# Optimization experiments

Hardware: AMD Instinct MI355X
Metric: run time of the kernel (lower is better)

## Reference

```python
import jax, jax.numpy as jnp
import numpy as np

N_EMBD = 1024
N_HEAD = 16
HEAD = N_EMBD // N_HEAD
B, T = 4, 2048


def setup_inputs() -> dict:
    key = jax.random.key(0)
    k1, k2, k3, k4, k5 = jax.random.split(key, 5)
    s = 1.0 / np.sqrt(N_EMBD)
    x = jax.random.normal(k1, (B, T, N_EMBD), dtype=jnp.float32)
    W_qkv = jax.random.uniform(k2, (N_EMBD, 3 * N_EMBD), jnp.float32, -s, s)
    b_qkv = jax.random.uniform(k3, (3 * N_EMBD,), jnp.float32, -s, s)
    W_out = jax.random.uniform(k4, (N_EMBD, N_EMBD), jnp.float32, -s, s)
    b_out = jax.random.uniform(k5, (N_EMBD,), jnp.float32, -s, s)
    return {"x": x, "W_qkv": W_qkv, "b_qkv": b_qkv, "W_out": W_out, "b_out": b_out}


def reference(x, W_qkv, b_qkv, W_out, b_out):
    Bx, Tx, C = x.shape
    qkv = x @ W_qkv + b_qkv                      # [B,T,3C]
    q, k, v = jnp.split(qkv, 3, axis=-1)
    def to_heads(t):
        return t.reshape(Bx, Tx, N_HEAD, HEAD).transpose(0, 2, 1, 3)  # [B,H,T,hd]
    q, k, v = to_heads(q), to_heads(k), to_heads(v)
    scores = jnp.einsum('bhqd,bhkd->bhqk', q, k) / np.sqrt(HEAD)
    causal = jnp.tril(jnp.ones((Tx, Tx), dtype=bool))
    scores = jnp.where(causal[None, None, :, :], scores, jnp.float32(-1e9))
    attn = jax.nn.softmax(scores, axis=-1)       # dropout p=0 (eval)
    out = jnp.einsum('bhqk,bhkd->bhqd', attn, v)
    out = out.transpose(0, 2, 1, 3).reshape(Bx, Tx, C)
    return out @ W_out + b_out
```

## Files before the change

### kernel.cpp

```cpp
#include <hip/hip_runtime.h>

typedef __attribute__((ext_vector_type(8))) short short8;
typedef __attribute__((ext_vector_type(8))) _Float16 half8;
typedef __attribute__((ext_vector_type(4))) float f32x4;
typedef __attribute__((ext_vector_type(16))) float f32x16;

#define MFMA_BF16(a, b, c) __builtin_amdgcn_mfma_f32_16x16x32_bf16(a, b, c, 0, 0, 0)
#define MFMA32_BF16(a, b, c) __builtin_amdgcn_mfma_f32_32x32x16_bf16(a, b, c, 0, 0, 0)
#define MFMA32_F16(a, b, c) __builtin_amdgcn_mfma_f32_32x32x16_f16(a, b, c, 0, 0, 0)

#define GLD16(g, l)                                                          \
  __builtin_amdgcn_global_load_lds(                                          \
      (const __attribute__((address_space(1))) unsigned int*)(g),            \
      (__attribute__((address_space(3))) unsigned int*)(l), 16, 0, 0)

__device__ __forceinline__ unsigned short f2bf(float f) {
  unsigned int u = __float_as_uint(f);
  u += 0x7fffu + ((u >> 16) & 1u);
  return (unsigned short)(u >> 16);
}

__global__ __launch_bounds__(256) void cvt_f32_bf16_k(const float* __restrict__ in,
                                                      unsigned short* __restrict__ out,
                                                      int n4) {
  int i = blockIdx.x * 256 + threadIdx.x;
  if (i < n4) {
    float4 v = reinterpret_cast<const float4*>(in)[i];
    ushort4 o;
    o.x = f2bf(v.x); o.y = f2bf(v.y); o.z = f2bf(v.z); o.w = f2bf(v.w);
    reinterpret_cast<ushort4*>(out)[i] = o;
  }
}

__global__ __launch_bounds__(256) void transpose_cvt_k(const float* __restrict__ W,
                                                       unsigned short* __restrict__ Wt,
                                                       int N) {
  __shared__ float tile[64][65];
  const int tid = threadIdx.x;
  const int tk = blockIdx.x * 64;
  const int tn = blockIdx.y * 64;
#pragma unroll
  for (int c = 0; c < 4; ++c) {
    int k = c * 16 + (tid >> 4);
    int n = (tid & 15) * 4;
    float4 v = *reinterpret_cast<const float4*>(&W[(size_t)(tk + k) * N + tn + n]);
    tile[k][n] = v.x; tile[k][n + 1] = v.y; tile[k][n + 2] = v.z; tile[k][n + 3] = v.w;
  }
  __syncthreads();
#pragma unroll
  for (int p = 0; p < 2; ++p) {
    int n = p * 32 + (tid >> 3);
    int k = (tid & 7) * 8;
    ushort4 a, b;
    a.x = f2bf(tile[k + 0][n]); a.y = f2bf(tile[k + 1][n]);
    a.z = f2bf(tile[k + 2][n]); a.w = f2bf(tile[k + 3][n]);
    b.x = f2bf(tile[k + 4][n]); b.y = f2bf(tile[k + 5][n]);
    b.z = f2bf(tile[k + 6][n]); b.w = f2bf(tile[k + 7][n]);
    *reinterpret_cast<ushort4*>(&Wt[(size_t)(tn + n) * 1024 + tk + k]) = a;
    *reinterpret_cast<ushort4*>(&Wt[(size_t)(tn + n) * 1024 + tk + k + 4]) = b;
  }
}

template <int MODE, int BN>
__global__ __launch_bounds__(256) void gemm_bt(const unsigned short* __restrict__ A,
                                               const unsigned short* __restrict__ Bt,
                                               const float* __restrict__ bias,
                                               float* __restrict__ outF,
                                               unsigned short* __restrict__ q_ws,
                                               unsigned short* __restrict__ k_ws,
                                               unsigned short* __restrict__ vt_ws,
                                               int M, int N, int K) {
  constexpr int NJ = BN / 32;
  constexpr int NBC = BN * 64 / 2048;
  __shared__ unsigned short As[128 * 64];
  __shared__ unsigned short Bs[BN * 64];

  const int tid = threadIdx.x;
  const int wave = tid >> 6, lane = tid & 63;
  const int quad = lane >> 4, l15 = lane & 15;
  const int m0 = blockIdx.x * 128, n0 = blockIdx.y * BN;
  const int wm = (wave & 1) * 64, wn = (wave >> 1) * (BN / 2);

  const f32x4 zf = {0.f, 0.f, 0.f, 0.f};
  f32x4 acc[4][NJ];
#pragma unroll
  for (int i = 0; i < 4; ++i)
#pragma unroll
    for (int j = 0; j < NJ; ++j) acc[i][j] = zf;

  const int rr = tid >> 3;
  const int scol = ((tid & 7) ^ (rr & 7)) * 8;
  const int swz = l15 & 7;

  for (int kt = 0; kt < K; kt += 64) {
    __syncthreads();
#pragma unroll
    for (int c = 0; c < 4; ++c)
      GLD16(&A[(size_t)(m0 + c * 32 + rr) * K + kt + scol], &As[c * 2048 + tid * 8]);
#pragma unroll
    for (int c = 0; c < NBC; ++c)
      GLD16(&Bt[(size_t)(n0 + c * 32 + rr) * K + kt + scol], &Bs[c * 2048 + tid * 8]);
    __syncthreads();

#pragma unroll
    for (int kk = 0; kk < 2; ++kk) {
      const int ch = (kk * 4 + quad) ^ swz;
      short8 af[4], bg[NJ];
#pragma unroll
      for (int i = 0; i < 4; ++i)
        af[i] = *reinterpret_cast<const short8*>(&As[(wm + i * 16 + l15) * 64 + ch * 8]);
#pragma unroll
      for (int j = 0; j < NJ; ++j)
        bg[j] = *reinterpret_cast<const short8*>(&Bs[(wn + j * 16 + l15) * 64 + ch * 8]);
#pragma unroll
      for (int i = 0; i < 4; ++i)
#pragma unroll
        for (int j = 0; j < NJ; ++j) acc[i][j] = MFMA_BF16(af[i], bg[j], acc[i][j]);
    }
  }

  const float kScQ = 0.125f * 1.44269504088896f;
  const int cls = n0 >> 10;
#pragma unroll
  for (int i = 0; i < 4; ++i) {
#pragma unroll
    for (int j = 0; j < NJ; ++j) {
      const int n = n0 + wn + j * 16 + l15;
      const float bv = bias[n];
      const int mb = m0 + wm + i * 16 + quad * 4;
      if (MODE == 1) {
#pragma unroll
        for (int r = 0; r < 4; ++r) outF[(size_t)(mb + r) * N + n] = acc[i][j][r] + bv;
      } else if (cls == 0) {
        const int b = mb >> 11, t0 = mb & 2047;
        const int h = n >> 6, d = n & 63;
#pragma unroll
        for (int r = 0; r < 4; ++r)
          q_ws[(((size_t)(b * 16 + h)) * 2048 + t0 + r) * 64 + d] =
              f2bf((acc[i][j][r] + bv) * kScQ);
      } else if (cls == 1) {
        const int b = mb >> 11, t0 = mb & 2047;
        const int n2 = n - 1024, h = n2 >> 6, d = n2 & 63;
#pragma unroll
        for (int r = 0; r < 4; ++r)
          k_ws[(((size_t)(b * 16 + h)) * 2048 + t0 + r) * 64 + d] = f2bf(acc[i][j][r] + bv);
      } else {
        const int b = mb >> 11, t0 = mb & 2047;
        const int n2 = n - 2048, h = n2 >> 6, d = n2 & 63;
        uint2 pk;
        pk.x = __builtin_bit_cast(unsigned int,
                                  __builtin_amdgcn_cvt_pkrtz(acc[i][j][0] + bv, acc[i][j][1] + bv));
        pk.y = __builtin_bit_cast(unsigned int,
                                  __builtin_amdgcn_cvt_pkrtz(acc[i][j][2] + bv, acc[i][j][3] + bv));
        *reinterpret_cast<uint2*>(
            &vt_ws[(((size_t)(b * 16 + h)) * 64 + d) * 2048 + t0]) = pk;
      }
    }
  }
}

__global__ __launch_bounds__(256, 3) void attn_k(const unsigned short* __restrict__ q_ws,
                                                 const unsigned short* __restrict__ k_ws,
                                                 const unsigned short* __restrict__ vt_ws,
                                                 unsigned short* __restrict__ att_ws) {
  const int T = 2048;
  const int bid = blockIdx.x;
  const int bh = (bid & 7) * 8 + ((bid >> 3) & 7);
  const int s = 15 - (bid >> 6);
  const int tid = threadIdx.x;
  const int wv = tid >> 6, lane = tid & 63;
  const int L = lane & 31, hl = lane >> 5;

  const unsigned short* Qh = q_ws + (size_t)bh * T * 64;
  const unsigned short* Kh = k_ws + (size_t)bh * T * 64;
  const _Float16* Vh = (const _Float16*)vt_ws + (size_t)bh * 64 * T;
  const int b = bh >> 4, h = bh & 15;

  __shared__ unsigned short Ks[2][64 * 64];
  __shared__ _Float16 Vs[2][64 * 64];
  __shared__ _Float16 plds_all[4][32 * 72];
  _Float16* plds = plds_all[wv];

  const int qw = s * 4 + wv;
  const int q0 = qw * 32;
  const int diagTile = qw >> 1;
  const int nk = 2 * s + 2;
  const int myq = q0 + L;

  short8 qb[4];
#pragma unroll
  for (int kk = 0; kk < 4; ++kk)
    qb[kk] = *reinterpret_cast<const short8*>(&Qh[(size_t)(q0 + L) * 64 + kk * 16 + hl * 8]);

  f32x16 o0 = {}, o1 = {};
  float l_i = 0.f;

  const int srow8 = tid >> 3;
  const int schunk = (tid & 7) ^ (srow8 & 7);

  GLD16(&Kh[(size_t)srow8 * 64 + schunk * 8], &Ks[0][tid * 8]);
  GLD16(&Kh[(size_t)(32 + srow8) * 64 + schunk * 8], &Ks[0][2048 + tid * 8]);
  GLD16(&Vh[(size_t)srow8 * T + schunk * 8], &Vs[0][tid * 8]);
  GLD16(&Vh[(size_t)(32 + srow8) * T + schunk * 8], &Vs[0][2048 + tid * 8]);

  for (int kt = 0; kt < nk; ++kt) {
    const int cur = kt & 1, nxt = cur ^ 1;
    if (kt) asm volatile("s_barrier" ::: "memory");
    const int pf = (kt + 1 < nk) ? kt + 1 : nk - 1;
    GLD16(&Kh[(size_t)(pf * 64 + srow8) * 64 + schunk * 8], &Ks[nxt][tid * 8]);
    GLD16(&Kh[(size_t)(pf * 64 + 32 + srow8) * 64 + schunk * 8], &Ks[nxt][2048 + tid * 8]);
    GLD16(&Vh[(size_t)srow8 * T + pf * 64 + schunk * 8], &Vs[nxt][tid * 8]);
    GLD16(&Vh[(size_t)(32 + srow8) * T + pf * 64 + schunk * 8], &Vs[nxt][2048 + tid * 8]);
    asm volatile("s_waitcnt vmcnt(4)\n\ts_barrier" ::: "memory");

    if (kt <= diagTile) {
      const unsigned short* KsC = Ks[cur];
      const _Float16* VsC = Vs[cur];
      const int kb = kt * 64;

      f32x16 sc0 = {}, sc1 = {};
#pragma unroll
      for (int kk = 0; kk < 4; ++kk) {
        const int sl = ((kk * 2 + hl) ^ (L & 7)) * 8;
        short8 k0 = *reinterpret_cast<const short8*>(&KsC[L * 64 + sl]);
        short8 k1 = *reinterpret_cast<const short8*>(&KsC[(32 + L) * 64 + sl]);
        sc0 = MFMA32_BF16(k0, qb[kk], sc0);
        sc1 = MFMA32_BF16(k1, qb[kk], sc1);
      }
      if (kt == diagTile) {
#pragma unroll
        for (int reg = 0; reg < 16; ++reg) {
          const int row = (reg & 3) + 8 * (reg >> 2) + 4 * hl;
          sc0[reg] = (kb + row > myq) ? -1e30f : sc0[reg];
          sc1[reg] = (kb + 32 + row > myq) ? -1e30f : sc1[reg];
        }
      }
#pragma unroll
      for (int c = 0; c < 2; ++c) {
        const f32x16& scc = c ? sc1 : sc0;
#pragma unroll
        for (int g = 0; g < 4; ++g) {
          float a0 = exp2f(scc[4 * g + 0]);
          float a1 = exp2f(scc[4 * g + 1]);
          float a2 = exp2f(scc[4 * g + 2]);
          float a3 = exp2f(scc[4 * g + 3]);
          l_i += (a0 + a1) + (a2 + a3);
          uint2 pk;
          pk.x = __builtin_bit_cast(unsigned int, __builtin_amdgcn_cvt_pkrtz(a0, a1));
          pk.y = __builtin_bit_cast(unsigned int, __builtin_amdgcn_cvt_pkrtz(a2, a3));
          *reinterpret_cast<uint2*>(&plds[L * 72 + c * 32 + g * 8 + hl * 4]) = pk;
        }
      }
      asm volatile("" ::: "memory");

#pragma unroll
      for (int t = 0; t < 4; ++t) {
        half8 pb = *reinterpret_cast<const half8*>(&plds[L * 72 + t * 16 + hl * 8]);
        const int sl = ((t * 2 + hl) ^ (L & 7)) * 8;
        half8 v0 = *reinterpret_cast<const half8*>(&VsC[L * 64 + sl]);
        half8 v1 = *reinterpret_cast<const half8*>(&VsC[(32 + L) * 64 + sl]);
        o0 = MFMA32_F16(v0, pb, o0);
        o1 = MFMA32_F16(v1, pb, o1);
      }
      asm volatile("" ::: "memory");
    }
  }
  asm volatile("s_waitcnt vmcnt(0)" ::: "memory");

  l_i += __shfl_xor(l_i, 32);
  const float inv = 1.f / l_i;
#pragma unroll
  for (int sg = 0; sg < 2; ++sg) {
    const f32x16& oo = sg ? o1 : o0;
#pragma unroll
    for (int g = 0; g < 4; ++g) {
      const int d0 = sg * 32 + g * 8 + hl * 4;
      uint2 ov;
      ov.x = (unsigned)f2bf(oo[4 * g + 0] * inv) | ((unsigned)f2bf(oo[4 * g + 1] * inv) << 16);
      ov.y = (unsigned)f2bf(oo[4 * g + 2] * inv) | ((unsigned)f2bf(oo[4 * g + 3] * inv) << 16);
      *reinterpret_cast<uint2*>(
          &att_ws[(size_t)(b * 2048 + q0 + L) * 1024 + h * 64 + d0]) = ov;
    }
  }
}

extern "C" void kernel_launch(void* const* d_in, const int* in_sizes, int n_in,
                              void* d_out, int out_size, void* d_ws, size_t ws_size,
                              hipStream_t stream) {
  (void)in_sizes; (void)n_in; (void)out_size; (void)ws_size;
  const float* x     = (const float*)d_in[0];
  const float* W_qkv = (const float*)d_in[1];
  const float* b_qkv = (const float*)d_in[2];
  const float* W_out = (const float*)d_in[3];
  const float* b_out = (const float*)d_in[4];
  float* out = (float*)d_out;

  char* ws = (char*)d_ws;
  unsigned short* xb    = (unsigned short*)(ws);
  unsigned short* wqkvT = (unsigned short*)(ws + 16777216);
  unsigned short* woutT = (unsigned short*)(ws + 23068672);
  unsigned short* q_ws  = (unsigned short*)(ws + 25165824);
  unsigned short* k_ws  = (unsigned short*)(ws + 41943040);
  unsigned short* vt_ws = (unsigned short*)(ws + 58720256);
  unsigned short* attb  = (unsigned short*)(ws + 75497472);

  cvt_f32_bf16_k<<<8192, 256, 0, stream>>>(x, xb, 2097152);
  transpose_cvt_k<<<dim3(16, 48), 256, 0, stream>>>(W_qkv, wqkvT, 3072);
  transpose_cvt_k<<<dim3(16, 16), 256, 0, stream>>>(W_out, woutT, 1024);

  dim3 g1(64, 24);
  gemm_bt<0, 128><<<g1, 256, 0, stream>>>(xb, wqkvT, b_qkv, nullptr, q_ws, k_ws, vt_ws,
                                          8192, 3072, 1024);
  attn_k<<<1024, 256, 0, stream>>>(q_ws, k_ws, vt_ws, attb);

  dim3 g2(64, 16);
  gemm_bt<1, 64><<<g2, 256, 0, stream>>>(attb, woutT, b_out, out, nullptr, nullptr, nullptr,
                                         8192, 1024, 1024);
}
```

Measured before the change: 243.0 us.

## Double-buffer GEMM K-loop and replace attention P LDS roundtrip with permlane swaps

The GEMM now uses double-buffered LDS tiles with a K-step of 32. The next tile's global-to-LDS load is issued before computing on the current tile, synchronised with vmcnt waits and raw barriers, and launch bounds ask for 4 blocks per CU. In attention, the probability matrix no longer goes through a per-wave LDS scratch buffer. It is rearranged in registers with v_permlane32_swap to form the MFMA B operand, which frees LDS and allows 4 blocks per CU. The risks are tighter register budgets from the raised occupancy target and fragile hand-written vmcnt counts. The smaller K tile also drops the XOR swizzle, which may add LDS bank conflicts.

Result: slower. 255.2 us (+5.0%).

```diff
diff --git a/kernel.cpp b/kernel.cpp
--- a/kernel.cpp
+++ b/kernel.cpp
@@ -4,6 +4,7 @@
 typedef __attribute__((ext_vector_type(8))) _Float16 half8;
 typedef __attribute__((ext_vector_type(4))) float f32x4;
 typedef __attribute__((ext_vector_type(16))) float f32x16;
+typedef __attribute__((ext_vector_type(4))) unsigned int u32x4;
 
 #define MFMA_BF16(a, b, c) __builtin_amdgcn_mfma_f32_16x16x32_bf16(a, b, c, 0, 0, 0)
 #define MFMA32_BF16(a, b, c) __builtin_amdgcn_mfma_f32_32x32x16_bf16(a, b, c, 0, 0, 0)
@@ -62,18 +63,18 @@
 }
 
 template <int MODE, int BN>
-__global__ __launch_bounds__(256) void gemm_bt(const unsigned short* __restrict__ A,
-                                               const unsigned short* __restrict__ Bt,
-                                               const float* __restrict__ bias,
-                                               float* __restrict__ outF,
-                                               unsigned short* __restrict__ q_ws,
-                                               unsigned short* __restrict__ k_ws,
-                                               unsigned short* __restrict__ vt_ws,
-                                               int M, int N, int K) {
+__global__ __launch_bounds__(256, 4) void gemm_bt(const unsigned short* __restrict__ A,
+                                                  const unsigned short* __restrict__ Bt,
+                                                  const float* __restrict__ bias,
+                                                  float* __restrict__ outF,
+                                                  unsigned short* __restrict__ q_ws,
+                                                  unsigned short* __restrict__ k_ws,
+                                                  unsigned short* __restrict__ vt_ws,
+                                                  int M, int N, int K) {
   constexpr int NJ = BN / 32;
-  constexpr int NBC = BN * 64 / 2048;
-  __shared__ unsigned short As[128 * 64];
-  __shared__ unsigned short Bs[BN * 64];
+  constexpr int NBG = BN / 64;
+  __shared__ unsigned short As[2][128 * 32];
+  __shared__ unsigned short Bs[2][BN * 32];
 
   const int tid = threadIdx.x;
   const int wave = tid >> 6, lane = tid & 63;
@@ -88,36 +89,45 @@
 #pragma unroll
     for (int j = 0; j < NJ; ++j) acc[i][j] = zf;
 
-  const int rr = tid >> 3;
-  const int scol = ((tid & 7) ^ (rr & 7)) * 8;
-  const int swz = l15 & 7;
-
-  for (int kt = 0; kt < K; kt += 64) {
-    __syncthreads();
-#pragma unroll
-    for (int c = 0; c < 4; ++c)
-      GLD16(&A[(size_t)(m0 + c * 32 + rr) * K + kt + scol], &As[c * 2048 + tid * 8]);
-#pragma unroll
-    for (int c = 0; c < NBC; ++c)
-      GLD16(&Bt[(size_t)(n0 + c * 32 + rr) * K + kt + scol], &Bs[c * 2048 + tid * 8]);
-    __syncthreads();
-
-#pragma unroll
-    for (int kk = 0; kk < 2; ++kk) {
-      const int ch = (kk * 4 + quad) ^ swz;
-      short8 af[4], bg[NJ];
-#pragma unroll
-      for (int i = 0; i < 4; ++i)
-        af[i] = *reinterpret_cast<const short8*>(&As[(wm + i * 16 + l15) * 64 + ch * 8]);
-#pragma unroll
-      for (int j = 0; j < NJ; ++j)
-        bg[j] = *reinterpret_cast<const short8*>(&Bs[(wn + j * 16 + l15) * 64 + ch * 8]);
-#pragma unroll
-      for (int i = 0; i < 4; ++i)
-#pragma unroll
-        for (int j = 0; j < NJ; ++j) acc[i][j] = MFMA_BF16(af[i], bg[j], acc[i][j]);
-    }
-  }
+  const int srow = tid >> 2;
+  const int scol = (tid & 3) * 8;
+
+#pragma unroll
+  for (int g = 0; g < 2; ++g)
+    GLD16(&A[(size_t)(m0 + g * 64 + srow) * K + scol], &As[0][g * 2048 + tid * 8]);
+#pragma unroll
+  for (int g = 0; g < NBG; ++g)
+    GLD16(&Bt[(size_t)(n0 + g * 64 + srow) * K + scol], &Bs[0][g * 2048 + tid * 8]);
+
+  const int nkt = K >> 5;
+  for (int kt = 0; kt < nkt; ++kt) {
+    const int cur = kt & 1, nxt = cur ^ 1;
+    if (kt) asm volatile("s_barrier" ::: "memory");
+    const int pofs = ((kt + 1 < nkt) ? kt + 1 : kt) * 32;
+#pragma unroll
+    for (int g = 0; g < 2; ++g)
+      GLD16(&A[(size_t)(m0 + g * 64 + srow) * K + pofs + scol], &As[nxt][g * 2048 + tid * 8]);
+#pragma unroll
+    for (int g = 0; g < NBG; ++g)
+      GLD16(&Bt[(size_t)(n0 + g * 64 + srow) * K + pofs + scol], &Bs[nxt][g * 2048 + tid * 8]);
+    if (NBG == 2)
+      asm volatile("s_waitcnt vmcnt(4)\n\ts_barrier" ::: "memory");
+    else
+      asm volatile("s_waitcnt vmcnt(3)\n\ts_barrier" ::: "memory");
+
+    short8 af[4], bg[NJ];
+#pragma unroll
+    for (int i = 0; i < 4; ++i)
+      af[i] = *reinterpret_cast<const short8*>(&As[cur][(wm + i * 16 + l15) * 32 + quad * 8]);
+#pragma unroll
+    for (int j = 0; j < NJ; ++j)
+      bg[j] = *reinterpret_cast<const short8*>(&Bs[cur][(wn + j * 16 + l15) * 32 + quad * 8]);
+#pragma unroll
+    for (int i = 0; i < 4; ++i)
+#pragma unroll
+      for (int j = 0; j < NJ; ++j) acc[i][j] = MFMA_BF16(af[i], bg[j], acc[i][j]);
+  }
+  asm volatile("s_waitcnt vmcnt(0)" ::: "memory");
 
   const float kScQ = 0.125f * 1.44269504088896f;
   const int cls = n0 >> 10;
@@ -159,7 +169,7 @@
   }
 }
 
-__global__ __launch_bounds__(256, 3) void attn_k(const unsigned short* __restrict__ q_ws,
+__global__ __launch_bounds__(256, 4) void attn_k(const unsigned short* __restrict__ q_ws,
                                                  const unsigned short* __restrict__ k_ws,
                                                  const unsigned short* __restrict__ vt_ws,
                                                  unsigned short* __restrict__ att_ws) {
@@ -178,8 +188,6 @@
 
   __shared__ unsigned short Ks[2][64 * 64];
   __shared__ _Float16 Vs[2][64 * 64];
-  __shared__ _Float16 plds_all[4][32 * 72];
-  _Float16* plds = plds_all[wv];
 
   const int qw = s * 4 + wv;
   const int q0 = qw * 32;
@@ -235,34 +243,36 @@
           sc1[reg] = (kb + 32 + row > myq) ? -1e30f : sc1[reg];
         }
       }
+      unsigned int qp[16];
 #pragma unroll
       for (int c = 0; c < 2; ++c) {
         const f32x16& scc = c ? sc1 : sc0;
 #pragma unroll
-        for (int g = 0; g < 4; ++g) {
-          float a0 = exp2f(scc[4 * g + 0]);
-          float a1 = exp2f(scc[4 * g + 1]);
-          float a2 = exp2f(scc[4 * g + 2]);
-          float a3 = exp2f(scc[4 * g + 3]);
-          l_i += (a0 + a1) + (a2 + a3);
-          uint2 pk;
-          pk.x = __builtin_bit_cast(unsigned int, __builtin_amdgcn_cvt_pkrtz(a0, a1));
-          pk.y = __builtin_bit_cast(unsigned int, __builtin_amdgcn_cvt_pkrtz(a2, a3));
-          *reinterpret_cast<uint2*>(&plds[L * 72 + c * 32 + g * 8 + hl * 4]) = pk;
+        for (int g = 0; g < 8; ++g) {
+          float a0 = exp2f(scc[2 * g]);
+          float a1 = exp2f(scc[2 * g + 1]);
+          l_i += a0 + a1;
+          qp[c * 8 + g] =
+              __builtin_bit_cast(unsigned int, __builtin_amdgcn_cvt_pkrtz(a0, a1));
         }
       }
-      asm volatile("" ::: "memory");
-
 #pragma unroll
       for (int t = 0; t < 4; ++t) {
-        half8 pb = *reinterpret_cast<const half8*>(&plds[L * 72 + t * 16 + hl * 8]);
+        asm volatile("v_permlane32_swap_b32 %0, %1"
+                     : "+v"(qp[4 * t + 0]), "+v"(qp[4 * t + 2]));
+        asm volatile("v_permlane32_swap_b32 %0, %1"
+                     : "+v"(qp[4 * t + 1]), "+v"(qp[4 * t + 3]));
+      }
+#pragma unroll
+      for (int t = 0; t < 4; ++t) {
+        u32x4 bu = {qp[4 * t + 0], qp[4 * t + 1], qp[4 * t + 2], qp[4 * t + 3]};
+        half8 pb = __builtin_bit_cast(half8, bu);
         const int sl = ((t * 2 + hl) ^ (L & 7)) * 8;
         half8 v0 = *reinterpret_cast<const half8*>(&VsC[L * 64 + sl]);
         half8 v1 = *reinterpret_cast<const half8*>(&VsC[(32 + L) * 64 + sl]);
         o0 = MFMA32_F16(v0, pb, o0);
         o1 = MFMA32_F16(v1, pb, o1);
       }
-      asm volatile("" ::: "memory");
     }
   }
   asm volatile("s_waitcnt vmcnt(0)" ::: "memory");
```
